# Kernel tuning notes

Hardware: AMD Instinct MI355X
Metric: run time of the kernel (lower is better)

## Reference

```python
import jax, jax.numpy as jnp
import numpy as np

B, S, D, H, HD, FF, W = 2, 4096, 2048, 16, 128, 8192, 256
EPS = 1e-6
ROPE_BASE = 10000.0


def rmsnorm(x, w):
    return x * jax.lax.rsqrt(jnp.mean(x * x, axis=-1, keepdims=True) + EPS) * w


def apply_rope(x):
    # x: [B, H, S, hd]
    hd = x.shape[-1]
    inv = 1.0 / (ROPE_BASE ** (jnp.arange(0, hd, 2, dtype=jnp.float32) / hd))
    ang = jnp.arange(x.shape[2], dtype=jnp.float32)[:, None] * inv[None, :]  # [S, hd/2]
    cos, sin = jnp.cos(ang), jnp.sin(ang)
    x1, x2 = jnp.split(x, 2, axis=-1)
    return jnp.concatenate([x1 * cos - x2 * sin, x1 * sin + x2 * cos], axis=-1)


def setup_inputs() -> dict:
    key = jax.random.key(0)
    ks = jax.random.split(key, 12)
    sc = 0.02
    return {
        "x": jax.random.normal(ks[0], (B, S, D), jnp.float32),
        "Wq": jax.random.normal(ks[1], (D, D), jnp.float32) * sc,
        "Wk": jax.random.normal(ks[2], (D, D), jnp.float32) * sc,
        "Wv": jax.random.normal(ks[3], (D, D), jnp.float32) * sc,
        "Wo": jax.random.normal(ks[4], (D, D), jnp.float32) * sc,
        "qn_w": jnp.ones((HD,), jnp.float32),
        "kn_w": jnp.ones((HD,), jnp.float32),
        "sink_logit": jax.random.normal(ks[5], (H,), jnp.float32) * sc,
        "attn_norm_w": jnp.ones((D,), jnp.float32),
        "ffn_norm_w": jnp.ones((D,), jnp.float32),
        "Wg": jax.random.normal(ks[6], (D, FF), jnp.float32) * sc,
        "Wu": jax.random.normal(ks[7], (D, FF), jnp.float32) * sc,
        "Wd": jax.random.normal(ks[8], (FF, D), jnp.float32) * sc,
    }


def reference(x, Wq, Wk, Wv, Wo, qn_w, kn_w, sink_logit, attn_norm_w, ffn_norm_w, Wg, Wu, Wd):
    # ---- sliding-window attention sublayer ----
    h = rmsnorm(x, attn_norm_w)
    q = (h @ Wq).reshape(B, S, H, HD)
    k = (h @ Wk).reshape(B, S, H, HD)
    v = (h @ Wv).reshape(B, S, H, HD)
    q = rmsnorm(q, qn_w)
    k = rmsnorm(k, kn_w)
    q = apply_rope(q.transpose(0, 2, 1, 3))  # [B,H,S,hd]
    k = apply_rope(k.transpose(0, 2, 1, 3))
    v = v.transpose(0, 2, 1, 3)

    nb = S // W
    qb = q.reshape(B, H, nb, W, HD)
    kb = k.reshape(B, H, nb, W, HD)
    vb = v.reshape(B, H, nb, W, HD)
    # each query block attends to previous block + own block (window=W causal)
    kprev = jnp.concatenate([jnp.zeros_like(kb[:, :, :1]), kb[:, :, :-1]], axis=2)
    vprev = jnp.concatenate([jnp.zeros_like(vb[:, :, :1]), vb[:, :, :-1]], axis=2)
    kl = jnp.concatenate([kprev, kb], axis=3)  # [B,H,nb,2W,hd]
    vl = jnp.concatenate([vprev, vb], axis=3)

    qi = jnp.arange(W)
    kj = jnp.arange(2 * W)
    rel = W + qi[:, None] - kj[None, :]  # q_pos - kv_pos within block pair
    base = (rel >= 0) & (rel < W)  # causal + in-window, [W, 2W]
    blk = jnp.arange(nb)
    kv_pos_valid = (blk[:, None, None] * W - W + kj[None, None, :]) >= 0  # [nb,1,2W]
    mask = base[None, :, :] & kv_pos_valid  # [nb, W, 2W]

    scale = 1.0 / jnp.sqrt(jnp.float32(HD))
    scores = jnp.einsum("bhnqd,bhnkd->bhnqk", qb, kl) * scale
    scores = jnp.where(mask[None, None], scores, jnp.float32(-1e30))
    # attention sink: virtual kv slot 0 with per-head logit, zero value
    sink = jnp.broadcast_to(sink_logit.reshape(1, H, 1, 1, 1), scores.shape[:-1] + (1,))
    logits = jnp.concatenate([sink, scores], axis=-1)
    p = jax.nn.softmax(logits, axis=-1)
    out = jnp.einsum("bhnqk,bhnkd->bhnqd", p[..., 1:], vl)  # sink contributes 0
    out = out.reshape(B, H, S, HD).transpose(0, 2, 1, 3).reshape(B, S, D)
    x = x + out @ Wo

    # ---- SwiGLU FFN sublayer ----
    h2 = rmsnorm(x, ffn_norm_w)
    x = x + (jax.nn.silu(h2 @ Wg) * (h2 @ Wu)) @ Wd
    return x
```

## Files before the change

### kernel.cpp

```cpp
#include <hip/hip_runtime.h>
#include <hip/hip_bf16.h>
#include <stdint.h>

typedef __bf16 bf16_t;
typedef __bf16 bf16x8 __attribute__((ext_vector_type(8)));
typedef float f32x4 __attribute__((ext_vector_type(4)));

#define B_ 2
#define S_ 4096
#define D_ 2048
#define H_ 16
#define HD_ 128
#define FF_ 8192
#define W_ 256
#define NB_ 16
#define ROWS_ 8192

__device__ __forceinline__ bool det_bf16(const uint32_t* det) {
  return (det[0] & 0xFFFFu) == 0x3F80u;
}
__device__ __forceinline__ float ldS(const void* p, size_t i, bool isbf) {
  return isbf ? (float)((const bf16_t*)p)[i] : ((const float*)p)[i];
}
__device__ __forceinline__ void ld8(const void* p, size_t i, bool isbf,
                                    float* f) {
  if (isbf) {
    bf16x8 v = *(const bf16x8*)((const bf16_t*)p + i);
#pragma unroll
    for (int j = 0; j < 8; ++j) f[j] = (float)v[j];
  } else {
    const float* s = (const float*)p + i;
    float4 a = *(const float4*)s;
    float4 b = *(const float4*)(s + 4);
    f[0] = a.x; f[1] = a.y; f[2] = a.z; f[3] = a.w;
    f[4] = b.x; f[5] = b.y; f[6] = b.z; f[7] = b.w;
  }
}

__device__ __forceinline__ void gld_lds16(const bf16_t* g, bf16_t* l) {
  __builtin_amdgcn_global_load_lds(
      (const __attribute__((address_space(1))) uint32_t*)g,
      (__attribute__((address_space(3))) uint32_t*)l, 16, 0, 0);
}

__global__ __launch_bounds__(256)
void transpose_k(const void* __restrict__ src, bf16_t* __restrict__ dst,
                 int R, int C, const uint32_t* __restrict__ det) {
  __shared__ __align__(16) bf16_t tile[64][72];
  const bool isbf = det_bf16(det);
  const int nbc = C >> 6;
  const int br = blockIdx.x / nbc, bc = blockIdx.x % nbc;
  const int t = threadIdx.x;
#pragma unroll
  for (int rnd = 0; rnd < 2; ++rnd) {
    int chunk = t + rnd * 256;
    int r = chunk >> 3;
    int c8 = (chunk & 7) << 3;
    float f[8];
    ld8(src, (size_t)(br * 64 + r) * C + bc * 64 + c8, isbf, f);
    union { bf16_t e[8]; int4 v; } u;
#pragma unroll
    for (int j = 0; j < 8; ++j) u.e[j] = (bf16_t)f[j];
    *(int4*)&tile[r][c8] = u.v;
  }
  __syncthreads();
#pragma unroll
  for (int rnd = 0; rnd < 2; ++rnd) {
    int chunk = t + rnd * 256;
    int cc = chunk >> 3;
    int r8 = (chunk & 7) << 3;
    union { bf16_t e[8]; int4 v; } u;
#pragma unroll
    for (int j = 0; j < 8; ++j) u.e[j] = tile[r8 + j][cc];
    *(int4*)&dst[(size_t)(bc * 64 + cc) * R + br * 64 + r8] = u.v;
  }
}

__global__ __launch_bounds__(256)
void rmsnorm_in_k(const void* __restrict__ x, const void* __restrict__ w,
                  bf16_t* __restrict__ out, const uint32_t* __restrict__ det) {
  __shared__ float sm[4];
  const bool isbf = det_bf16(det);
  const size_t row = blockIdx.x;
  const int i0 = threadIdx.x << 3;
  float f[8], ss = 0.f;
  ld8(x, row * D_ + i0, isbf, f);
#pragma unroll
  for (int j = 0; j < 8; ++j) ss += f[j] * f[j];
#pragma unroll
  for (int off = 1; off < 64; off <<= 1) ss += __shfl_xor(ss, off, 64);
  if ((threadIdx.x & 63) == 0) sm[threadIdx.x >> 6] = ss;
  __syncthreads();
  float tot = sm[0] + sm[1] + sm[2] + sm[3];
  float rs = rsqrtf(tot * (1.0f / D_) + 1e-6f);
  float wf[8];
  ld8(w, i0, isbf, wf);
  bf16x8 res;
#pragma unroll
  for (int j = 0; j < 8; ++j) res[j] = (bf16_t)(f[j] * rs * wf[j]);
  *(bf16x8*)&out[row * D_ + i0] = res;
}

__global__ __launch_bounds__(256)
void rmsnorm_f32_k(const float* __restrict__ x, const void* __restrict__ w,
                   bf16_t* __restrict__ out, const uint32_t* __restrict__ det) {
  __shared__ float sm[4];
  const bool isbf = det_bf16(det);
  const size_t row = blockIdx.x;
  const int i0 = threadIdx.x << 3;
  float4 a = *(const float4*)&x[row * D_ + i0];
  float4 b = *(const float4*)&x[row * D_ + i0 + 4];
  float f[8] = {a.x, a.y, a.z, a.w, b.x, b.y, b.z, b.w};
  float ss = 0.f;
#pragma unroll
  for (int j = 0; j < 8; ++j) ss += f[j] * f[j];
#pragma unroll
  for (int off = 1; off < 64; off <<= 1) ss += __shfl_xor(ss, off, 64);
  if ((threadIdx.x & 63) == 0) sm[threadIdx.x >> 6] = ss;
  __syncthreads();
  float tot = sm[0] + sm[1] + sm[2] + sm[3];
  float rs = rsqrtf(tot * (1.0f / D_) + 1e-6f);
  float wf[8];
  ld8(w, i0, isbf, wf);
  bf16x8 res;
#pragma unroll
  for (int j = 0; j < 8; ++j) res[j] = (bf16_t)(f[j] * rs * wf[j]);
  *(bf16x8*)&out[row * D_ + i0] = res;
}

__global__ __launch_bounds__(256)
void qknorm_rope_k(bf16_t* __restrict__ q, bf16_t* __restrict__ k,
                   const void* __restrict__ qw, const void* __restrict__ kw,
                   const uint32_t* __restrict__ det) {
  const bool isbf = det_bf16(det);
  const int wv = threadIdx.x >> 6;
  const int i = threadIdx.x & 63;
  const int idx = blockIdx.x * 4 + wv;
  const int s = (idx >> 4) & (S_ - 1);
  const size_t base = (size_t)idx * HD_;

  float inv = exp2f((float)i * -0.20762050593046014f);
  float ang = (float)s * inv;
  float sn, cs;
  sincosf(ang, &sn, &cs);

#pragma unroll
  for (int t = 0; t < 2; ++t) {
    bf16_t* p = (t == 0) ? (q + base) : (k + base);
    const void* w = (t == 0) ? qw : kw;
    float x1 = (float)p[i], x2 = (float)p[i + 64];
    float ss = x1 * x1 + x2 * x2;
#pragma unroll
    for (int off = 1; off < 64; off <<= 1) ss += __shfl_xor(ss, off, 64);
    float rs = rsqrtf(ss * (1.0f / HD_) + 1e-6f);
    float n1 = x1 * rs * ldS(w, i, isbf);
    float n2 = x2 * rs * ldS(w, i + 64, isbf);
    p[i] = (bf16_t)(n1 * cs - n2 * sn);
    p[i + 64] = (bf16_t)(n1 * sn + n2 * cs);
  }
}

#define T256 (256 * 64)

template <int EPI>
__global__ __launch_bounds__(512)
void gemm256_k(const bf16_t* __restrict__ A, const bf16_t* __restrict__ Bt,
               void* __restrict__ C, const void* __restrict__ aux,
               const uint32_t* __restrict__ det, int M, int N, int K) {
  extern __shared__ __align__(16) bf16_t lds[];
  bf16_t* bufA = lds;
  bf16_t* bufB = lds + 2 * T256;

  bool isbf = false;
  if constexpr (EPI == 1 || EPI == 3) isbf = det_bf16(det);

  const int tid = threadIdx.x;
  const int lane = tid & 63, wid = tid >> 6;
  const int l15 = lane & 15, l4 = lane >> 4;
  const int wm = wid >> 2, wn = wid & 3;

  const int nwg = gridDim.x;
  const int nbm = M >> 8;
  const int orig = blockIdx.x;
  const int q8 = nwg >> 3, r8 = nwg & 7, xcd = orig & 7;
  const int swz = (xcd < r8 ? xcd * (q8 + 1) : r8 * (q8 + 1) + (xcd - r8) * q8)
                + (orig >> 3);
  const int bm = swz % nbm;
  const int bn = swz / nbm;

  const bf16_t* Ag = A + (size_t)(bm * 256) * K;
  const bf16_t* Bg = Bt + (size_t)(bn * 256) * K;

  auto stage = [&](const bf16_t* g, int k0, bf16_t* lb) {
#pragma unroll
    for (int j = 0; j < 4; ++j) {
      int c = j * 512 + tid;
      int row = c >> 3, u = c & 7;
      int col = k0 + ((u ^ (row & 7)) << 3);
      gld_lds16(g + (size_t)row * K + col, lb + c * 8);
    }
  };

  stage(Ag, 0, bufA);
  stage(Bg, 0, bufB);
  stage(Ag, 64, bufA + T256);
  stage(Bg, 64, bufB + T256);
  asm volatile("s_waitcnt vmcnt(8)" ::: "memory");
  asm volatile("s_barrier" ::: "memory");

  const int nt = K >> 6;
  f32x4 acc[8][4] = {};

  for (int t = 0; t < nt; ++t) {
    const bf16_t* a = bufA + (t & 1) * T256;
    const bf16_t* b = bufB + (t & 1) * T256;

    bf16x8 bfr[4][2];
#pragma unroll
    for (int n = 0; n < 4; ++n)
#pragma unroll
      for (int ks = 0; ks < 2; ++ks) {
        int R = wn * 64 + n * 16 + l15;
        bfr[n][ks] = *(const bf16x8*)&b[R * 64 + ((((ks << 2) | l4) ^ (R & 7)) << 3)];
      }
#pragma unroll
    for (int mh = 0; mh < 2; ++mh) {
      bf16x8 af[4][2];
#pragma unroll
      for (int m = 0; m < 4; ++m)
#pragma unroll
        for (int ks = 0; ks < 2; ++ks) {
          int R = wm * 128 + mh * 64 + m * 16 + l15;
          af[m][ks] = *(const bf16x8*)&a[R * 64 + ((((ks << 2) | l4) ^ (R & 7)) << 3)];
        }
      __builtin_amdgcn_s_setprio(1);
#pragma unroll
      for (int m = 0; m < 4; ++m)
#pragma unroll
        for (int n = 0; n < 4; ++n)
#pragma unroll
          for (int ks = 0; ks < 2; ++ks)
            acc[mh * 4 + m][n] = __builtin_amdgcn_mfma_f32_16x16x32_bf16(
                af[m][ks], bfr[n][ks], acc[mh * 4 + m][n], 0, 0, 0);
      __builtin_amdgcn_s_setprio(0);
    }

    asm volatile("s_barrier" ::: "memory");
    if (t + 2 < nt) {
      int k0 = (t + 2) << 6;
      stage(Ag, k0, bufA + (t & 1) * T256);
      stage(Bg, k0, bufB + (t & 1) * T256);
      asm volatile("s_waitcnt vmcnt(8)" ::: "memory");
    } else {
      asm volatile("s_waitcnt vmcnt(0)" ::: "memory");
    }
    asm volatile("s_barrier" ::: "memory");
  }

#pragma unroll
  for (int m8 = 0; m8 < 8; ++m8) {
#pragma unroll
    for (int r = 0; r < 4; ++r) {
      const int row = bm * 256 + wm * 128 + m8 * 16 + l4 * 4 + r;
#pragma unroll
      for (int n = 0; n < 4; ++n) {
        const int col = bn * 256 + wn * 64 + n * 16 + l15;
        const size_t idx = (size_t)row * N + col;
        const float val = acc[m8][n][r];
        if constexpr (EPI == 0) {
          ((bf16_t*)C)[idx] = (bf16_t)val;
        } else if constexpr (EPI == 1) {
          ((float*)C)[idx] = ldS(aux, idx, isbf) + val;
        } else if constexpr (EPI == 2) {
          float g = (float)((const bf16_t*)aux)[idx];
          float sg = g / (1.f + __expf(-g));
          ((bf16_t*)C)[idx] = (bf16_t)(sg * val);
        } else {
          float v = ((const float*)aux)[idx] + val;
          if (isbf) ((bf16_t*)C)[idx] = (bf16_t)v;
          else      ((float*)C)[idx] = v;
        }
      }
    }
  }
}

__global__ __launch_bounds__(512)
void attn_k(const bf16_t* __restrict__ Q, const bf16_t* __restrict__ K,
            const bf16_t* __restrict__ V, const void* __restrict__ sink,
            bf16_t* __restrict__ O, const uint32_t* __restrict__ det) {
  __shared__ __align__(16) bf16_t Ks[64][128];
  __shared__ __align__(16) bf16_t Vt[128][64];
  __shared__ __align__(16) bf16_t Ps[8][32][64];

  const bool isbf = det_bf16(det);
  const int bx = blockIdx.x;
  const int n = bx & (NB_ - 1);
  const int h = (bx >> 4) & (H_ - 1);
  const int b = bx >> 8;
  const int tid = threadIdx.x;
  const int wv = tid >> 6, lane = tid & 63;
  const int l15 = lane & 15, l4 = lane >> 4;
  const size_t headbase = ((size_t)b * S_ * H_ + h) * HD_;
  const int RS = H_ * HD_;
  const int q0 = n * W_;
  const int wq = wv * 32;

  bf16x8 qf[2][4];
#pragma unroll
  for (int mi = 0; mi < 2; ++mi)
#pragma unroll
    for (int kb = 0; kb < 4; ++kb) {
      int s = q0 + wq + mi * 16 + l15;
      qf[mi][kb] = *(const bf16x8*)&Q[headbase + (size_t)s * RS + kb * 32 + l4 * 8];
    }

  const float sinkl = ldS(sink, h, isbf);
  float m_run[2][4], l_run[2][4];
#pragma unroll
  for (int mi = 0; mi < 2; ++mi)
#pragma unroll
    for (int r = 0; r < 4; ++r) { m_run[mi][r] = sinkl; l_run[mi][r] = 1.0f; }
  f32x4 oacc[2][8] = {};

  const int kvbase = q0 - W_;
  const float scale = 0.088388347648318447f;

  for (int c = 0; c < 8; ++c) {
    __syncthreads();
#pragma unroll
    for (int rnd = 0; rnd < 2; ++rnd) {
      int chunk = tid + rnd * 512;
      int r = chunk >> 4;
      int c8 = (chunk & 15) << 3;
      int sk = kvbase + c * 64 + r;
      int4 kv = {0, 0, 0, 0}, vvv = {0, 0, 0, 0};
      if (sk >= 0) {
        kv = *(const int4*)&K[headbase + (size_t)sk * RS + c8];
        vvv = *(const int4*)&V[headbase + (size_t)sk * RS + c8];
      }
      *(int4*)&Ks[r][c8] = kv;
      const bf16_t* pv = (const bf16_t*)&vvv;
#pragma unroll
      for (int j = 0; j < 8; ++j) Vt[c8 + j][r] = pv[j];
    }
    __syncthreads();

    bool any = (c * 64 + 63 >= wq + 1) && (c * 64 <= wq + 31 + W_);
    if (n == 0 && c < 4) any = false;
    if (!any) continue;

    f32x4 sacc[2][4] = {};
#pragma unroll
    for (int kb = 0; kb < 4; ++kb) {
      bf16x8 kf[4];
#pragma unroll
      for (int ni = 0; ni < 4; ++ni)
        kf[ni] = *(const bf16x8*)&Ks[ni * 16 + l15][kb * 32 + l4 * 8];
#pragma unroll
      for (int mi = 0; mi < 2; ++mi)
#pragma unroll
        for (int ni = 0; ni < 4; ++ni)
          sacc[mi][ni] = __builtin_amdgcn_mfma_f32_16x16x32_bf16(
              qf[mi][kb], kf[ni], sacc[mi][ni], 0, 0, 0);
    }

#pragma unroll
    for (int mi = 0; mi < 2; ++mi) {
#pragma unroll
      for (int r = 0; r < 4; ++r) {
        const int qi = wq + mi * 16 + l4 * 4 + r;
        float mx = -3.0e38f;
#pragma unroll
        for (int ni = 0; ni < 4; ++ni) {
          int kj = c * 64 + ni * 16 + l15;
          bool ok = (kj > qi) && (kj <= qi + W_) && (n > 0 || kj >= W_);
          float sv = ok ? sacc[mi][ni][r] * scale : -1.0e30f;
          sacc[mi][ni][r] = sv;
          mx = fmaxf(mx, sv);
        }
#pragma unroll
        for (int off = 1; off < 16; off <<= 1)
          mx = fmaxf(mx, __shfl_xor(mx, off, 64));
        float mo = m_run[mi][r];
        float mn = fmaxf(mo, mx);
        float alpha = __expf(mo - mn);
        m_run[mi][r] = mn;
        float rs = 0.f;
#pragma unroll
        for (int ni = 0; ni < 4; ++ni) {
          float p = __expf(sacc[mi][ni][r] - mn);
          sacc[mi][ni][r] = p;
          rs += p;
        }
#pragma unroll
        for (int off = 1; off < 16; off <<= 1) rs += __shfl_xor(rs, off, 64);
        l_run[mi][r] = l_run[mi][r] * alpha + rs;
#pragma unroll
        for (int ni = 0; ni < 8; ++ni) oacc[mi][ni][r] *= alpha;
      }
    }

#pragma unroll
    for (int mi = 0; mi < 2; ++mi)
#pragma unroll
      for (int ni = 0; ni < 4; ++ni)
#pragma unroll
        for (int r = 0; r < 4; ++r)
          Ps[wv][mi * 16 + l4 * 4 + r][ni * 16 + l15] = (bf16_t)sacc[mi][ni][r];

#pragma unroll
    for (int kb2 = 0; kb2 < 2; ++kb2) {
      bf16x8 pf[2];
#pragma unroll
      for (int mi = 0; mi < 2; ++mi)
        pf[mi] = *(const bf16x8*)&Ps[wv][mi * 16 + l15][kb2 * 32 + l4 * 8];
#pragma unroll
      for (int ni = 0; ni < 8; ++ni) {
        bf16x8 vf = *(const bf16x8*)&Vt[ni * 16 + l15][kb2 * 32 + l4 * 8];
#pragma unroll
        for (int mi = 0; mi < 2; ++mi)
          oacc[mi][ni] = __builtin_amdgcn_mfma_f32_16x16x32_bf16(
              pf[mi], vf, oacc[mi][ni], 0, 0, 0);
      }
    }
  }

#pragma unroll
  for (int mi = 0; mi < 2; ++mi)
#pragma unroll
    for (int r = 0; r < 4; ++r) {
      float inv = 1.0f / l_run[mi][r];
      int s = q0 + wq + mi * 16 + l4 * 4 + r;
#pragma unroll
      for (int ni = 0; ni < 8; ++ni)
        O[headbase + (size_t)s * RS + ni * 16 + l15] =
            (bf16_t)(oacc[mi][ni][r] * inv);
    }
}

extern "C" void kernel_launch(void* const* d_in, const int* in_sizes, int n_in,
                              void* d_out, int out_size, void* d_ws,
                              size_t ws_size, hipStream_t stream) {
  const void* x   = d_in[0];
  const void* Wq  = d_in[1];
  const void* Wk  = d_in[2];
  const void* Wv  = d_in[3];
  const void* Wo  = d_in[4];
  const void* qnw = d_in[5];
  const void* knw = d_in[6];
  const void* snk = d_in[7];
  const void* anw = d_in[8];
  const void* fnw = d_in[9];
  const void* Wg  = d_in[10];
  const void* Wu  = d_in[11];
  const void* Wd  = d_in[12];
  const uint32_t* det = (const uint32_t*)anw;

  char* ws = (char*)d_ws;
  const size_t MB = 1024ull * 1024ull;
  bf16_t* WT = (bf16_t*)(ws + 0 * MB);
  bf16_t* hb = (bf16_t*)(ws + 32 * MB);
  bf16_t* qb = (bf16_t*)(ws + 64 * MB);
  bf16_t* kb = (bf16_t*)(ws + 96 * MB);
  bf16_t* vb = (bf16_t*)(ws + 128 * MB);
  bf16_t* ao = (bf16_t*)(ws + 160 * MB);
  float* xm  = (float*)(ws + 192 * MB);
  bf16_t* gb = (bf16_t*)(ws + 64 * MB);

  const int LDSZ = 131072;
  hipFuncSetAttribute((const void*)gemm256_k<0>,
                      hipFuncAttributeMaxDynamicSharedMemorySize, LDSZ);
  hipFuncSetAttribute((const void*)gemm256_k<1>,
                      hipFuncAttributeMaxDynamicSharedMemorySize, LDSZ);
  hipFuncSetAttribute((const void*)gemm256_k<2>,
                      hipFuncAttributeMaxDynamicSharedMemorySize, LDSZ);
  hipFuncSetAttribute((const void*)gemm256_k<3>,
                      hipFuncAttributeMaxDynamicSharedMemorySize, LDSZ);

  rmsnorm_in_k<<<ROWS_, 256, 0, stream>>>(x, anw, hb, det);

  transpose_k<<<32 * 32, 256, 0, stream>>>(Wq, WT, 2048, 2048, det);
  gemm256_k<0><<<32 * 8, 512, LDSZ, stream>>>(hb, WT, qb, nullptr, det, 8192, 2048, 2048);
  transpose_k<<<32 * 32, 256, 0, stream>>>(Wk, WT, 2048, 2048, det);
  gemm256_k<0><<<32 * 8, 512, LDSZ, stream>>>(hb, WT, kb, nullptr, det, 8192, 2048, 2048);
  transpose_k<<<32 * 32, 256, 0, stream>>>(Wv, WT, 2048, 2048, det);
  gemm256_k<0><<<32 * 8, 512, LDSZ, stream>>>(hb, WT, vb, nullptr, det, 8192, 2048, 2048);

  qknorm_rope_k<<<B_ * S_ * H_ / 4, 256, 0, stream>>>(qb, kb, qnw, knw, det);

  attn_k<<<B_ * H_ * NB_, 512, 0, stream>>>(qb, kb, vb, snk, ao, det);

  transpose_k<<<32 * 32, 256, 0, stream>>>(Wo, WT, 2048, 2048, det);
  gemm256_k<1><<<32 * 8, 512, LDSZ, stream>>>(ao, WT, xm, x, det, 8192, 2048, 2048);

  rmsnorm_f32_k<<<ROWS_, 256, 0, stream>>>(xm, fnw, hb, det);

  transpose_k<<<32 * 128, 256, 0, stream>>>(Wg, WT, 2048, 8192, det);
  gemm256_k<0><<<32 * 32, 512, LDSZ, stream>>>(hb, WT, gb, nullptr, det, 8192, 8192, 2048);
  transpose_k<<<32 * 128, 256, 0, stream>>>(Wu, WT, 2048, 8192, det);
  gemm256_k<2><<<32 * 32, 512, LDSZ, stream>>>(hb, WT, gb, gb, det, 8192, 8192, 2048);
  transpose_k<<<128 * 32, 256, 0, stream>>>(Wd, WT, 8192, 2048, det);
  gemm256_k<3><<<32 * 8, 512, LDSZ, stream>>>(gb, WT, d_out, xm, det, 8192, 2048, 8192);

  (void)in_sizes; (void)n_in; (void)out_size; (void)ws_size;
}
```

Before: 1.404 ms.

## Interleave GEMM global prefetch with quarter-tile MFMA phases in 8-wave schedule

Restructures the 256x256 GEMM main loop into an unrolled two-buffer schedule. Each K-tile is split into four MFMA quarters (A-half by B-half), and LDS fragment reads and async global-to-LDS loads for the next tiles are spread between those quarters with barriers. The aim is to hide global load latency and LDS read latency behind MFMA work, in the style of hand-scheduled ping-pong kernels. It adds many barriers per iteration, which could cost throughput, and it assumes K is a multiple of 128.

```diff
diff --git a/kernel.cpp b/kernel.cpp
--- a/kernel.cpp
+++ b/kernel.cpp
@@ -15,6 +15,9 @@
 #define W_ 256
 #define NB_ 16
 #define ROWS_ 8192
+
+#define BAR()   asm volatile("s_barrier" ::: "memory")
+#define LGKM0() asm volatile("s_waitcnt lgkmcnt(0)" ::: "memory")
 
 __device__ __forceinline__ bool det_bf16(const uint32_t* det) {
   return (det[0] & 0xFFFFu) == 0x3F80u;
@@ -168,8 +171,10 @@
                void* __restrict__ C, const void* __restrict__ aux,
                const uint32_t* __restrict__ det, int M, int N, int K) {
   extern __shared__ __align__(16) bf16_t lds[];
-  bf16_t* bufA = lds;
-  bf16_t* bufB = lds + 2 * T256;
+  bf16_t* A0 = lds;
+  bf16_t* A1 = lds + T256;
+  bf16_t* B0 = lds + 2 * T256;
+  bf16_t* B1 = lds + 3 * T256;
 
   bool isbf = false;
   if constexpr (EPI == 1 || EPI == 3) isbf = det_bf16(det);
@@ -191,70 +196,91 @@
   const bf16_t* Ag = A + (size_t)(bm * 256) * K;
   const bf16_t* Bg = Bt + (size_t)(bn * 256) * K;
 
-  auto stage = [&](const bf16_t* g, int k0, bf16_t* lb) {
-#pragma unroll
-    for (int j = 0; j < 4; ++j) {
-      int c = j * 512 + tid;
-      int row = c >> 3, u = c & 7;
-      int col = k0 + ((u ^ (row & 7)) << 3);
-      gld_lds16(g + (size_t)row * K + col, lb + c * 8);
-    }
+  const int st_r = tid >> 3;
+  const int st_u = tid & 7;
+  auto stq = [&](const bf16_t* g, int q, int k0, bf16_t* lb) {
+    int row = q * 64 + st_r;
+    int col = k0 + ((st_u ^ (st_r & 7)) << 3);
+    gld_lds16(g + (size_t)row * K + col, lb + row * 64 + st_u * 8);
   };
 
-  stage(Ag, 0, bufA);
-  stage(Bg, 0, bufB);
-  stage(Ag, 64, bufA + T256);
-  stage(Bg, 64, bufB + T256);
-  asm volatile("s_waitcnt vmcnt(8)" ::: "memory");
-  asm volatile("s_barrier" ::: "memory");
-
-  const int nt = K >> 6;
-  f32x4 acc[8][4] = {};
-
-  for (int t = 0; t < nt; ++t) {
-    const bf16_t* a = bufA + (t & 1) * T256;
-    const bf16_t* b = bufB + (t & 1) * T256;
-
-    bf16x8 bfr[4][2];
-#pragma unroll
-    for (int n = 0; n < 4; ++n)
+  bf16x8 af[4][2], bf0[2][2], bf1[2][2];
+  auto rdA = [&](const bf16_t* a, int qm) {
+#pragma unroll
+    for (int m = 0; m < 4; ++m)
 #pragma unroll
       for (int ks = 0; ks < 2; ++ks) {
-        int R = wn * 64 + n * 16 + l15;
+        int R = wm * 128 + qm * 64 + m * 16 + l15;
+        af[m][ks] = *(const bf16x8*)&a[R * 64 + ((((ks << 2) | l4) ^ (R & 7)) << 3)];
+      }
+  };
+  auto rdB = [&](const bf16_t* b, int qn, bf16x8 (*bfr)[2]) {
+#pragma unroll
+    for (int n = 0; n < 2; ++n)
+#pragma unroll
+      for (int ks = 0; ks < 2; ++ks) {
+        int R = wn * 64 + qn * 32 + n * 16 + l15;
         bfr[n][ks] = *(const bf16x8*)&b[R * 64 + ((((ks << 2) | l4) ^ (R & 7)) << 3)];
       }
-#pragma unroll
-    for (int mh = 0; mh < 2; ++mh) {
-      bf16x8 af[4][2];
-#pragma unroll
-      for (int m = 0; m < 4; ++m)
-#pragma unroll
-        for (int ks = 0; ks < 2; ++ks) {
-          int R = wm * 128 + mh * 64 + m * 16 + l15;
-          af[m][ks] = *(const bf16x8*)&a[R * 64 + ((((ks << 2) | l4) ^ (R & 7)) << 3)];
-        }
-      __builtin_amdgcn_s_setprio(1);
-#pragma unroll
-      for (int m = 0; m < 4; ++m)
-#pragma unroll
-        for (int n = 0; n < 4; ++n)
-#pragma unroll
-          for (int ks = 0; ks < 2; ++ks)
-            acc[mh * 4 + m][n] = __builtin_amdgcn_mfma_f32_16x16x32_bf16(
-                af[m][ks], bfr[n][ks], acc[mh * 4 + m][n], 0, 0, 0);
-      __builtin_amdgcn_s_setprio(0);
-    }
-
-    asm volatile("s_barrier" ::: "memory");
-    if (t + 2 < nt) {
-      int k0 = (t + 2) << 6;
-      stage(Ag, k0, bufA + (t & 1) * T256);
-      stage(Bg, k0, bufB + (t & 1) * T256);
-      asm volatile("s_waitcnt vmcnt(8)" ::: "memory");
-    } else {
-      asm volatile("s_waitcnt vmcnt(0)" ::: "memory");
-    }
-    asm volatile("s_barrier" ::: "memory");
+  };
+
+  f32x4 acc[8][4] = {};
+  auto mma = [&](bf16x8 (*bfr)[2], int qm, int qn) {
+    __builtin_amdgcn_s_setprio(1);
+#pragma unroll
+    for (int m = 0; m < 4; ++m)
+#pragma unroll
+      for (int n = 0; n < 2; ++n)
+#pragma unroll
+        for (int ks = 0; ks < 2; ++ks)
+          acc[qm * 4 + m][qn * 2 + n] = __builtin_amdgcn_mfma_f32_16x16x32_bf16(
+              af[m][ks], bfr[n][ks], acc[qm * 4 + m][qn * 2 + n], 0, 0, 0);
+    __builtin_amdgcn_s_setprio(0);
+  };
+
+#pragma unroll
+  for (int q = 0; q < 4; ++q) { stq(Ag, q, 0, A0); stq(Bg, q, 0, B0); }
+#pragma unroll
+  for (int q = 0; q < 4; ++q) { stq(Ag, q, 64, A1); stq(Bg, q, 64, B1); }
+  asm volatile("s_waitcnt vmcnt(8)" ::: "memory");
+  BAR();
+
+  const int NI = K >> 7;
+  int k2 = 128;
+  for (int it = 0; it < NI; ++it) {
+    const bool pf = (it + 1 < NI);
+
+    rdA(A0, 0); rdB(B0, 0, bf0);
+    BAR(); LGKM0(); mma(bf0, 0, 0); BAR();
+    rdB(B0, 1, bf1);
+    if (pf) { stq(Ag, 0, k2, A0); stq(Ag, 2, k2, A0); }
+    BAR(); LGKM0(); mma(bf1, 0, 1); BAR();
+    rdA(A0, 1);
+    if (pf) { stq(Bg, 0, k2, B0); stq(Bg, 1, k2, B0); }
+    BAR(); LGKM0(); mma(bf0, 1, 0); BAR();
+    if (pf) { stq(Bg, 2, k2, B0); stq(Bg, 3, k2, B0);
+              stq(Ag, 1, k2, A0); stq(Ag, 3, k2, A0); }
+    BAR(); LGKM0(); mma(bf1, 1, 1);
+    if (pf) { asm volatile("s_waitcnt vmcnt(8)" ::: "memory"); }
+    else    { asm volatile("s_waitcnt vmcnt(0)" ::: "memory"); }
+    BAR();
+
+    rdA(A1, 0); rdB(B1, 0, bf0);
+    BAR(); LGKM0(); mma(bf0, 0, 0); BAR();
+    rdB(B1, 1, bf1);
+    if (pf) { stq(Ag, 0, k2 + 64, A1); stq(Ag, 2, k2 + 64, A1); }
+    BAR(); LGKM0(); mma(bf1, 0, 1); BAR();
+    rdA(A1, 1);
+    if (pf) { stq(Bg, 0, k2 + 64, B1); stq(Bg, 1, k2 + 64, B1); }
+    BAR(); LGKM0(); mma(bf0, 1, 0); BAR();
+    if (pf) { stq(Bg, 2, k2 + 64, B1); stq(Bg, 3, k2 + 64, B1);
+              stq(Ag, 1, k2 + 64, A1); stq(Ag, 3, k2 + 64, A1); }
+    BAR(); LGKM0(); mma(bf1, 1, 1);
+    if (pf) { asm volatile("s_waitcnt vmcnt(8)" ::: "memory"); }
+    else    { asm volatile("s_waitcnt vmcnt(0)" ::: "memory"); }
+    BAR();
+
+    k2 += 128;
   }
 
 #pragma unroll
```

Result: no change. 1.391 ms (-0.9%).

## Restructure GEMM mainloop into 4-stage BK=32 ring with single barrier

Applied to the files above, without the earlier changes.

The 256x256 bf16 GEMM main loop now uses K-steps of 32 with a four-deep LDS ring buffer instead of K-steps of 64 with double buffering. Each iteration issues the next global-to-LDS prefetch before its MFMAs and needs only one barrier. LDS offsets are precomputed with a new XOR swizzle to cut per-iteration address math. The change also adds a min-2-blocks launch bound, which caps register use and could cause spills given the large accumulator tile, and it drops the s_setprio hints.

```diff
diff --git a/kernel.cpp b/kernel.cpp
--- a/kernel.cpp
+++ b/kernel.cpp
@@ -15,6 +15,8 @@
 #define W_ 256
 #define NB_ 16
 #define ROWS_ 8192
+
+#define BAR() asm volatile("s_barrier" ::: "memory")
 
 __device__ __forceinline__ bool det_bf16(const uint32_t* det) {
   return (det[0] & 0xFFFFu) == 0x3F80u;
@@ -160,16 +162,16 @@
   }
 }
 
-#define T256 (256 * 64)
+#define TQ 8192
 
 template <int EPI>
-__global__ __launch_bounds__(512)
+__global__ __launch_bounds__(512, 2)
 void gemm256_k(const bf16_t* __restrict__ A, const bf16_t* __restrict__ Bt,
                void* __restrict__ C, const void* __restrict__ aux,
                const uint32_t* __restrict__ det, int M, int N, int K) {
   extern __shared__ __align__(16) bf16_t lds[];
-  bf16_t* bufA = lds;
-  bf16_t* bufB = lds + 2 * T256;
+  bf16_t* Ab = lds;
+  bf16_t* Bb = lds + 4 * TQ;
 
   bool isbf = false;
   if constexpr (EPI == 1 || EPI == 3) isbf = det_bf16(det);
@@ -191,70 +193,68 @@
   const bf16_t* Ag = A + (size_t)(bm * 256) * K;
   const bf16_t* Bg = Bt + (size_t)(bn * 256) * K;
 
-  auto stage = [&](const bf16_t* g, int k0, bf16_t* lb) {
-#pragma unroll
-    for (int j = 0; j < 4; ++j) {
-      int c = j * 512 + tid;
-      int row = c >> 3, u = c & 7;
-      int col = k0 + ((u ^ (row & 7)) << 3);
-      gld_lds16(g + (size_t)row * K + col, lb + c * 8);
-    }
-  };
-
-  stage(Ag, 0, bufA);
-  stage(Bg, 0, bufB);
-  stage(Ag, 64, bufA + T256);
-  stage(Bg, 64, bufB + T256);
-  asm volatile("s_waitcnt vmcnt(8)" ::: "memory");
-  asm volatile("s_barrier" ::: "memory");
-
-  const int nt = K >> 6;
+  const int c0 = tid, c1 = 512 + tid;
+  const int r0 = c0 >> 2, r1 = c1 >> 2;
+  const size_t goff0 = (size_t)r0 * K + (((c0 & 3) ^ ((r0 >> 1) & 3)) << 3);
+  const size_t goff1 = (size_t)r1 * K + (((c1 & 3) ^ ((r1 >> 1) & 3)) << 3);
+  const int loff0 = c0 * 8, loff1 = c1 * 8;
+
+  int aoff[8], boff[4];
+#pragma unroll
+  for (int m = 0; m < 8; ++m) {
+    int R = wm * 128 + m * 16 + l15;
+    aoff[m] = R * 32 + ((l4 ^ ((R >> 1) & 3)) << 3);
+  }
+#pragma unroll
+  for (int n = 0; n < 4; ++n) {
+    int R = wn * 64 + n * 16 + l15;
+    boff[n] = R * 32 + ((l4 ^ ((R >> 1) & 3)) << 3);
+  }
+
   f32x4 acc[8][4] = {};
+  const int nt = K >> 5;
+
+  gld_lds16(Ag + goff0, Ab + loff0);
+  gld_lds16(Ag + goff1, Ab + loff1);
+  gld_lds16(Bg + goff0, Bb + loff0);
+  gld_lds16(Bg + goff1, Bb + loff1);
+  gld_lds16(Ag + 32 + goff0, Ab + TQ + loff0);
+  gld_lds16(Ag + 32 + goff1, Ab + TQ + loff1);
+  gld_lds16(Bg + 32 + goff0, Bb + TQ + loff0);
+  gld_lds16(Bg + 32 + goff1, Bb + TQ + loff1);
+  asm volatile("s_waitcnt vmcnt(4)" ::: "memory");
+  BAR();
 
   for (int t = 0; t < nt; ++t) {
-    const bf16_t* a = bufA + (t & 1) * T256;
-    const bf16_t* b = bufB + (t & 1) * T256;
-
-    bf16x8 bfr[4][2];
-#pragma unroll
-    for (int n = 0; n < 4; ++n)
-#pragma unroll
-      for (int ks = 0; ks < 2; ++ks) {
-        int R = wn * 64 + n * 16 + l15;
-        bfr[n][ks] = *(const bf16x8*)&b[R * 64 + ((((ks << 2) | l4) ^ (R & 7)) << 3)];
-      }
-#pragma unroll
-    for (int mh = 0; mh < 2; ++mh) {
-      bf16x8 af[4][2];
-#pragma unroll
-      for (int m = 0; m < 4; ++m)
-#pragma unroll
-        for (int ks = 0; ks < 2; ++ks) {
-          int R = wm * 128 + mh * 64 + m * 16 + l15;
-          af[m][ks] = *(const bf16x8*)&a[R * 64 + ((((ks << 2) | l4) ^ (R & 7)) << 3)];
-        }
-      __builtin_amdgcn_s_setprio(1);
-#pragma unroll
-      for (int m = 0; m < 4; ++m)
-#pragma unroll
-        for (int n = 0; n < 4; ++n)
-#pragma unroll
-          for (int ks = 0; ks < 2; ++ks)
-            acc[mh * 4 + m][n] = __builtin_amdgcn_mfma_f32_16x16x32_bf16(
-                af[m][ks], bfr[n][ks], acc[mh * 4 + m][n], 0, 0, 0);
-      __builtin_amdgcn_s_setprio(0);
-    }
-
-    asm volatile("s_barrier" ::: "memory");
+    const bf16_t* a = Ab + (t & 3) * TQ;
+    const bf16_t* b = Bb + (t & 3) * TQ;
+
+    bf16x8 af[8], bfr[4];
+#pragma unroll
+    for (int n = 0; n < 4; ++n) bfr[n] = *(const bf16x8*)&b[boff[n]];
+#pragma unroll
+    for (int m = 0; m < 8; ++m) af[m] = *(const bf16x8*)&a[aoff[m]];
+
     if (t + 2 < nt) {
-      int k0 = (t + 2) << 6;
-      stage(Ag, k0, bufA + (t & 1) * T256);
-      stage(Bg, k0, bufB + (t & 1) * T256);
-      asm volatile("s_waitcnt vmcnt(8)" ::: "memory");
-    } else {
-      asm volatile("s_waitcnt vmcnt(0)" ::: "memory");
-    }
-    asm volatile("s_barrier" ::: "memory");
+      bf16_t* la = Ab + ((t + 2) & 3) * TQ;
+      bf16_t* lb = Bb + ((t + 2) & 3) * TQ;
+      const size_t k0 = (size_t)(t + 2) << 5;
+      gld_lds16(Ag + k0 + goff0, la + loff0);
+      gld_lds16(Ag + k0 + goff1, la + loff1);
+      gld_lds16(Bg + k0 + goff0, lb + loff0);
+      gld_lds16(Bg + k0 + goff1, lb + loff1);
+    }
+
+#pragma unroll
+    for (int m = 0; m < 8; ++m)
+#pragma unroll
+      for (int n = 0; n < 4; ++n)
+        acc[m][n] = __builtin_amdgcn_mfma_f32_16x16x32_bf16(af[m], bfr[n],
+                                                            acc[m][n], 0, 0, 0);
+
+    if (t + 2 < nt) { asm volatile("s_waitcnt vmcnt(4)" ::: "memory"); }
+    else            { asm volatile("s_waitcnt vmcnt(0)" ::: "memory"); }
+    BAR();
   }
 
 #pragma unroll
```

Result: faster. 1.376 ms (-2.0%).
